# Optimization experiments

Measured on AMD Instinct MI355X. Metric: run time of the kernel, lower is better.

## Reference

```python
import jax, jax.numpy as jnp
import numpy as np

HIDDEN = 1280
HEADS = 8
RANK = 4
BATCH = 2
SEQ = 4096


def setup_inputs() -> dict:
    key = jax.random.key(0)
    ks = jax.random.split(key, 11)
    s = 1.0 / np.sqrt(HIDDEN)
    return {
        "hidden_states": jax.random.normal(ks[0], (BATCH, SEQ, HIDDEN), jnp.float32),
        # attn projections (stored as [in, out] for x @ W)
        "w_q": jax.random.normal(ks[1], (HIDDEN, HIDDEN), jnp.float32) * s,
        "w_k": jax.random.normal(ks[2], (HIDDEN, HIDDEN), jnp.float32) * s,
        "w_v": jax.random.normal(ks[3], (HIDDEN, HIDDEN), jnp.float32) * s,
        # LoRA down/up matrices for K and V
        "lora_k_a": jax.random.normal(ks[4], (HIDDEN, RANK), jnp.float32) * s,
        "lora_k_b": jax.random.normal(ks[5], (RANK, HIDDEN), jnp.float32) * 0.5,
        "lora_v_a": jax.random.normal(ks[6], (HIDDEN, RANK), jnp.float32) * s,
        "lora_v_b": jax.random.normal(ks[7], (RANK, HIDDEN), jnp.float32) * 0.5,
        # output projection (to_out[0]); to_out[1] is dropout -> identity at eval
        "w_out": jax.random.normal(ks[8], (HIDDEN, HIDDEN), jnp.float32) * s,
        "b_out": jax.random.normal(ks[9], (HIDDEN,), jnp.float32) * 0.01,
    }


def reference(hidden_states, w_q, w_k, w_v, lora_k_a, lora_k_b,
              lora_v_a, lora_v_b, w_out, b_out):
    B, S, D = hidden_states.shape
    H = HEADS
    dh = D // H
    scale = 1.0 / np.sqrt(dh)

    # QKV projections
    q = hidden_states @ w_q                      # [B, S, D]
    k = hidden_states @ w_k
    v = hidden_states @ w_v

    # LoRA low-rank residual updates to key/value
    k = k + (k @ lora_k_a) @ lora_k_b            # rank-4 update
    v = v + (v @ lora_v_a) @ lora_v_b

    # head_to_batch_dim: [B, S, D] -> [B, H, S, dh]
    q = q.reshape(B, S, H, dh).transpose(0, 2, 1, 3)
    k = k.reshape(B, S, H, dh).transpose(0, 2, 1, 3)
    v = v.reshape(B, S, H, dh).transpose(0, 2, 1, 3)

    # naive attention: scores -> softmax -> weighted sum
    scores = jnp.einsum("bhqd,bhkd->bhqk", q, k) * scale   # [B, H, S, S]
    probs = jax.nn.softmax(scores, axis=-1)
    out = jnp.einsum("bhqk,bhkd->bhqd", probs, v)          # [B, H, S, dh]

    # batch_to_head_dim: [B, H, S, dh] -> [B, S, D]
    out = out.transpose(0, 2, 1, 3).reshape(B, S, D)

    # to_out[0] linear; to_out[1] dropout is identity in eval
    return out @ w_out + b_out
```

## Files before the change

### kernel.cpp

```cpp
#include <hip/hip_runtime.h>
#include <stdint.h>

typedef __attribute__((ext_vector_type(8))) __bf16 bf16x8;
typedef __attribute__((ext_vector_type(2))) __bf16 bf16x2;
typedef __attribute__((ext_vector_type(4))) float f32x4;
typedef __attribute__((ext_vector_type(16))) float f32x16;
typedef unsigned short u16;

#define LOG2E 1.44269504088896f

static_assert(sizeof(bf16x8) == 16, "bf16x8 must be 16B");

__device__ __forceinline__ u16 f2bf(float f) {
  unsigned u = __builtin_bit_cast(unsigned, f);
  u += 0x7fffu + ((u >> 16) & 1u);
  return (u16)(u >> 16);
}

__device__ __forceinline__ void load_lds16(const void* g, void* l) {
  __builtin_amdgcn_global_load_lds((const __attribute__((address_space(1))) void*)g,
                                   (__attribute__((address_space(3))) void*)l, 16, 0, 0);
}

__global__ __launch_bounds__(256) void lora_tmp_k(
    const float* __restrict__ wk, const float* __restrict__ wv,
    const float* __restrict__ ka, const float* __restrict__ va,
    float* __restrict__ tk, float* __restrict__ tv) {
  const int i = blockIdx.x;
  const float* W = blockIdx.y ? wv : wk;
  const float* A = blockIdx.y ? va : ka;
  float* T = blockIdx.y ? tv : tk;
  float s0 = 0.f, s1 = 0.f, s2 = 0.f, s3 = 0.f;
  for (int j = threadIdx.x; j < 1280; j += 256) {
    float w = W[(size_t)i * 1280 + j];
    float4 a4 = *(const float4*)(A + (size_t)j * 4);
    s0 += w * a4.x; s1 += w * a4.y; s2 += w * a4.z; s3 += w * a4.w;
  }
#pragma unroll
  for (int m = 1; m < 64; m <<= 1) {
    s0 += __shfl_xor(s0, m); s1 += __shfl_xor(s1, m);
    s2 += __shfl_xor(s2, m); s3 += __shfl_xor(s3, m);
  }
  __shared__ float red[4][4];
  const int wv_ = threadIdx.x >> 6;
  if ((threadIdx.x & 63) == 0) {
    red[wv_][0] = s0; red[wv_][1] = s1; red[wv_][2] = s2; red[wv_][3] = s3;
  }
  __syncthreads();
  if (threadIdx.x < 4) {
    float r = red[0][threadIdx.x] + red[1][threadIdx.x] + red[2][threadIdx.x] + red[3][threadIdx.x];
    T[(size_t)i * 4 + threadIdx.x] = r;
  }
}

__global__ void wt_prep_k(const float* __restrict__ W, const float* __restrict__ tmp,
                          const float* __restrict__ LB, u16* __restrict__ WT) {
  __shared__ float tile[32][33];
  const int o0 = blockIdx.x * 32, i0 = blockIdx.y * 32;
  const int tx = threadIdx.x, ty = threadIdx.y;
#pragma unroll
  for (int kk = 0; kk < 4; ++kk) {
    int i = i0 + ty + kk * 8, o = o0 + tx;
    float v = W[(size_t)i * 1280 + o];
    if (tmp) {
      float4 t = *(const float4*)(tmp + (size_t)i * 4);
      v += t.x * LB[o] + t.y * LB[1280 + o] + t.z * LB[2560 + o] + t.w * LB[3840 + o];
    }
    tile[ty + kk * 8][tx] = v;
  }
  __syncthreads();
#pragma unroll
  for (int kk = 0; kk < 4; ++kk) {
    int o = o0 + ty + kk * 8, i = i0 + tx;
    WT[(size_t)o * 1280 + i] = f2bf(tile[tx][ty + kk * 8]);
  }
}

__global__ __launch_bounds__(256) void cvt_bf16_k(const float* __restrict__ in,
                                                  u16* __restrict__ out, int n4) {
  for (int i = blockIdx.x * 256 + threadIdx.x; i < n4; i += gridDim.x * 256) {
    float4 v = ((const float4*)in)[i];
    ushort4 o;
    o.x = f2bf(v.x); o.y = f2bf(v.y); o.z = f2bf(v.z); o.w = f2bf(v.w);
    ((ushort4*)out)[i] = o;
  }
}

__global__ void vtrans_k(const u16* __restrict__ V, u16* __restrict__ VT) {
  __shared__ u16 tile[32][33];
  const int s0 = blockIdx.x * 32, c0 = blockIdx.y * 32, b = blockIdx.z;
  const int tx = threadIdx.x, ty = threadIdx.y;
#pragma unroll
  for (int kk = 0; kk < 4; ++kk)
    tile[ty + kk * 8][tx] = V[(size_t)(b * 4096 + s0 + ty + kk * 8) * 1280 + c0 + tx];
  __syncthreads();
#pragma unroll
  for (int kk = 0; kk < 4; ++kk)
    VT[(size_t)(b * 1280 + c0 + ty + kk * 8) * 4096 + s0 + tx] = tile[tx][ty + kk * 8];
}

template <bool F32OUT>
__global__ __launch_bounds__(256) void gemm128_k(
    const u16* __restrict__ A, const u16* __restrict__ WT,
    void* __restrict__ outp, const float* __restrict__ bias, float oscale) {
  __shared__ __align__(16) u16 lds[2 * 128 * 40];
  u16* ldsA = lds;
  u16* ldsB = lds + 128 * 40;
  const int tid = threadIdx.x;
  const int lane = tid & 63, lrow = lane & 15, lhi = lane >> 4;
  const int w = tid >> 6, wm = w >> 1, wn = w & 1;
  const size_t M0 = (size_t)blockIdx.x * 128, N0 = (size_t)blockIdx.y * 128;
  const int wb = tid & 192;
  f32x4 acc[4][4] = {};

  for (int k0 = 0; k0 < 1280; k0 += 32) {
#pragma unroll
    for (int j = 0; j < 3; ++j) {
      if (j < 2 || tid < 128) {
        int i = j * 256 + tid;
        int row = i / 5, c = i % 5; c = c < 4 ? c : 3;
        load_lds16(A + (M0 + row) * 1280 + k0 + c * 8, ldsA + (j * 256 + wb) * 8);
      }
    }
#pragma unroll
    for (int j = 0; j < 3; ++j) {
      if (j < 2 || tid < 128) {
        int i = j * 256 + tid;
        int row = i / 5, c = i % 5; c = c < 4 ? c : 3;
        load_lds16(WT + (N0 + row) * 1280 + k0 + c * 8, ldsB + (j * 256 + wb) * 8);
      }
    }
    __syncthreads();
    bf16x8 af[4], bfr[4];
#pragma unroll
    for (int m = 0; m < 4; ++m)
      af[m] = *(const bf16x8*)(ldsA + (wm * 64 + m * 16 + lrow) * 40 + lhi * 8);
#pragma unroll
    for (int n = 0; n < 4; ++n)
      bfr[n] = *(const bf16x8*)(ldsB + (wn * 64 + n * 16 + lrow) * 40 + lhi * 8);
#pragma unroll
    for (int m = 0; m < 4; ++m)
#pragma unroll
      for (int n = 0; n < 4; ++n)
        acc[m][n] = __builtin_amdgcn_mfma_f32_16x16x32_bf16(af[m], bfr[n], acc[m][n], 0, 0, 0);
    __syncthreads();
  }

#pragma unroll
  for (int m = 0; m < 4; ++m)
#pragma unroll
    for (int n = 0; n < 4; ++n)
#pragma unroll
      for (int r = 0; r < 4; ++r) {
        size_t row = M0 + wm * 64 + m * 16 + lhi * 4 + r;
        size_t col = N0 + wn * 64 + n * 16 + lrow;
        float v = acc[m][n][r];
        if (F32OUT)
          ((float*)outp)[row * 1280 + col] = v + bias[col];
        else
          ((u16*)outp)[row * 1280 + col] = f2bf(v * oscale);
      }
}

__global__ __launch_bounds__(256, 2) void attn_k(
    const u16* __restrict__ Q, const u16* __restrict__ K,
    const u16* __restrict__ VT, u16* __restrict__ AO) {
  __shared__ __align__(16) u16 lds_all[34816];
  u16* const kb0 = lds_all;
  u16* const kb1 = lds_all + 12288;
  u16* const vt = lds_all + 24576;
  const int tid = threadIdx.x;
  const int lane = tid & 63;
  const int l31 = lane & 31, lhi5 = lane >> 5;
  const int lo32 = (lane < 32);
  const int w = tid >> 6;
  const int bh = blockIdx.x, qt = blockIdx.y;
  const int b = bh >> 3, h = bh & 7;
  const int wb = tid & 192;

  const u16* Kg = K + (size_t)b * 4096 * 1280 + h * 160;
  const u16* VTg = VT + ((size_t)b * 1280 + h * 160) * 4096;

  bf16x8 qf[10];
  const u16* Qg = Q + (size_t)(b * 4096 + qt * 128 + w * 32 + l31) * 1280 + h * 160 + lhi5 * 8;
#pragma unroll
  for (int kf = 0; kf < 10; ++kf) qf[kf] = *(const bf16x8*)(Qg + kf * 16);
#pragma unroll
  for (int kf = 0; kf < 10; ++kf) asm volatile("" : "+v"(qf[kf]));

  auto stageK = [&](int kv0, u16* dst) {
#pragma unroll
    for (int j = 0; j < 6; ++j) {
      int i = j * 256 + tid;
      int row = i / 24, cl = i % 24;
      int cg = (cl & 24) | ((cl ^ row) & 7);
      cg = cg < 20 ? cg : 19;
      load_lds16(Kg + (size_t)(kv0 + row) * 1280 + cg * 8, dst + (j * 256 + wb) * 8);
    }
  };
  auto stageV = [&](int kv0) {
#pragma unroll
    for (int j = 0; j < 5; ++j) {
      int i = j * 256 + tid;
      int row = i >> 3, cl = i & 7;
      int cg = cl ^ (row & 7);
      load_lds16(VTg + (size_t)row * 4096 + kv0 + cg * 8, vt + (j * 256 + wb) * 8);
    }
  };

  stageK(0, kb0);

  f32x16 o[5] = {};
  float m_run = -1e30f, l_run = 0.f;

  for (int t = 0; t < 64; ++t) {
    const u16* kcur = (t & 1) ? kb1 : kb0;
    u16* knext = (t & 1) ? kb0 : kb1;
    stageV(t * 64);
    if (t < 63) stageK((t + 1) * 64, knext);
    if (t < 63) { asm volatile("s_waitcnt vmcnt(11)" ::: "memory"); }
    else        { asm volatile("s_waitcnt vmcnt(5)" ::: "memory"); }
    __builtin_amdgcn_s_barrier();
    __builtin_amdgcn_sched_barrier(0);

    f32x16 sacc[2] = {};
    __builtin_amdgcn_s_setprio(1);
#pragma unroll
    for (int kf = 0; kf < 10; ++kf) {
      const int c = 2 * kf + lhi5;
#pragma unroll
      for (int mt = 0; mt < 2; ++mt) {
        const int row = mt * 32 + l31;
        const int slot = (c & 24) | ((c ^ row) & 7);
        bf16x8 ka = *(const bf16x8*)(kcur + row * 192 + slot * 8);
        sacc[mt] = __builtin_amdgcn_mfma_f32_32x32x16_bf16(ka, qf[kf], sacc[mt], 0, 0, 0);
      }
    }
    __builtin_amdgcn_s_setprio(0);

    float mx = -1e30f;
#pragma unroll
    for (int mt = 0; mt < 2; ++mt)
#pragma unroll
      for (int i = 0; i < 16; ++i) mx = fmaxf(mx, sacc[mt][i]);
    mx = fmaxf(mx, __shfl_xor(mx, 32));
    if (__any(mx - m_run > 8.0f)) {
      float mnew = fmaxf(m_run, mx);
      float al = __builtin_amdgcn_exp2f((m_run - mnew) * LOG2E);
      l_run *= al; m_run = mnew;
#pragma unroll
      for (int dm = 0; dm < 5; ++dm)
#pragma unroll
        for (int i = 0; i < 16; ++i) o[dm][i] *= al;
    }
    float rs = 0.f;
    unsigned xp[2][8];
#pragma unroll
    for (int mt = 0; mt < 2; ++mt)
#pragma unroll
      for (int r = 0; r < 8; ++r) {
        float p0 = __builtin_amdgcn_exp2f((sacc[mt][2 * r] - m_run) * LOG2E);
        float p1 = __builtin_amdgcn_exp2f((sacc[mt][2 * r + 1] - m_run) * LOG2E);
        rs += p0 + p1;
        bf16x2 pk; pk[0] = (__bf16)p0; pk[1] = (__bf16)p1;
        xp[mt][r] = __builtin_bit_cast(unsigned, pk);
      }
    rs += __shfl_xor(rs, 32);
    l_run += rs;

    if (t < 63) { asm volatile("s_waitcnt vmcnt(6)" ::: "memory"); }
    else        { asm volatile("s_waitcnt vmcnt(0)" ::: "memory"); }
    __builtin_amdgcn_s_barrier();
    __builtin_amdgcn_sched_barrier(0);

    __builtin_amdgcn_s_setprio(1);
#pragma unroll
    for (int kf = 0; kf < 4; ++kf) {
      const int mt = kf >> 1, hf = kf & 1;
      unsigned xa = xp[mt][hf * 4 + 0], xb = xp[mt][hf * 4 + 1];
      unsigned xc = xp[mt][hf * 4 + 2], xd = xp[mt][hf * 4 + 3];
      unsigned sa = __shfl_xor((int)xa, 32), sb = __shfl_xor((int)xb, 32);
      unsigned sc = __shfl_xor((int)xc, 32), sd = __shfl_xor((int)xd, 32);
      uint4 pw;
      pw.x = lo32 ? xa : sc;
      pw.y = lo32 ? xb : sd;
      pw.z = lo32 ? sa : xc;
      pw.w = lo32 ? sb : xd;
      bf16x8 pB = __builtin_bit_cast(bf16x8, pw);
      const int c = 2 * kf + lhi5;
#pragma unroll
      for (int dm = 0; dm < 5; ++dm) {
        const int row = dm * 32 + l31;
        bf16x8 va = *(const bf16x8*)(vt + row * 64 + ((c ^ (row & 7)) * 8));
        o[dm] = __builtin_amdgcn_mfma_f32_32x32x16_bf16(va, pB, o[dm], 0, 0, 0);
      }
    }
    __builtin_amdgcn_s_setprio(0);
    __builtin_amdgcn_sched_barrier(0);
    __builtin_amdgcn_s_barrier();
    __builtin_amdgcn_sched_barrier(0);
  }

  float invl = 1.f / l_run;
  u16* tr = lds_all + w * 5376;
#pragma unroll
  for (int dm = 0; dm < 5; ++dm)
#pragma unroll
    for (int k = 0; k < 4; ++k) {
      int d = dm * 32 + k * 8 + lhi5 * 4;
      unsigned lo_ = (unsigned)f2bf(o[dm][4 * k + 0] * invl) |
                     ((unsigned)f2bf(o[dm][4 * k + 1] * invl) << 16);
      unsigned hi_ = (unsigned)f2bf(o[dm][4 * k + 2] * invl) |
                     ((unsigned)f2bf(o[dm][4 * k + 3] * invl) << 16);
      uint2 u; u.x = lo_; u.y = hi_;
      *(uint2*)(tr + l31 * 168 + d) = u;
    }
  asm volatile("s_waitcnt lgkmcnt(0)" ::: "memory");
  __builtin_amdgcn_sched_barrier(0);
  const size_t qg0 = (size_t)(b * 4096 + qt * 128 + w * 32);
#pragma unroll
  for (int it = 0; it < 10; ++it) {
    int idx = it * 64 + lane;
    int row = idx / 20, cc = idx % 20;
    bf16x8 vch = *(const bf16x8*)(tr + row * 168 + cc * 8);
    *(bf16x8*)(AO + (qg0 + row) * 1280 + h * 160 + cc * 8) = vch;
  }
}

extern "C" void kernel_launch(void* const* d_in, const int* in_sizes, int n_in,
                              void* d_out, int out_size, void* d_ws, size_t ws_size,
                              hipStream_t stream) {
  const float* hs  = (const float*)d_in[0];
  const float* w_q = (const float*)d_in[1];
  const float* w_k = (const float*)d_in[2];
  const float* w_v = (const float*)d_in[3];
  const float* lka = (const float*)d_in[4];
  const float* lkb = (const float*)d_in[5];
  const float* lva = (const float*)d_in[6];
  const float* lvb = (const float*)d_in[7];
  const float* w_o = (const float*)d_in[8];
  const float* b_o = (const float*)d_in[9];
  float* out = (float*)d_out;
  char* ws = (char*)d_ws;

  const size_t KA  = 0;
  const size_t VA  = 20480;
  const size_t WTQ = 40960;
  const size_t WTK = WTQ + 3276800;
  const size_t WTV = WTK + 3276800;
  const size_t WTO = WTV + 3276800;
  const size_t HSB = WTO + 3276800;
  const size_t QB  = HSB + 20971520;
  const size_t KB  = QB + 20971520;
  const size_t VB  = KB + 20971520;
  const size_t VTB = VB + 20971520;
  const size_t AOB = VTB + 20971520;
  const size_t END = AOB + 20971520;
  if (ws_size < END) return;

  float* tk = (float*)(ws + KA);
  float* tv = (float*)(ws + VA);
  u16* wtq = (u16*)(ws + WTQ);
  u16* wtk = (u16*)(ws + WTK);
  u16* wtv = (u16*)(ws + WTV);
  u16* wto = (u16*)(ws + WTO);
  u16* hsb = (u16*)(ws + HSB);
  u16* qb  = (u16*)(ws + QB);
  u16* kb  = (u16*)(ws + KB);
  u16* vb  = (u16*)(ws + VB);
  u16* vtb = (u16*)(ws + VTB);
  u16* aob = (u16*)(ws + AOB);

  lora_tmp_k<<<dim3(1280, 2), 256, 0, stream>>>(w_k, w_v, lka, lva, tk, tv);
  wt_prep_k<<<dim3(40, 40), dim3(32, 8), 0, stream>>>(w_q, nullptr, nullptr, wtq);
  wt_prep_k<<<dim3(40, 40), dim3(32, 8), 0, stream>>>(w_k, tk, lkb, wtk);
  wt_prep_k<<<dim3(40, 40), dim3(32, 8), 0, stream>>>(w_v, tv, lvb, wtv);
  wt_prep_k<<<dim3(40, 40), dim3(32, 8), 0, stream>>>(w_o, nullptr, nullptr, wto);
  cvt_bf16_k<<<2048, 256, 0, stream>>>(hs, hsb, 2621440);

  const float qscale = 0.07905694150420949f;
  gemm128_k<false><<<dim3(64, 10), 256, 0, stream>>>(hsb, wtq, qb, nullptr, qscale);
  gemm128_k<false><<<dim3(64, 10), 256, 0, stream>>>(hsb, wtk, kb, nullptr, 1.0f);
  gemm128_k<false><<<dim3(64, 10), 256, 0, stream>>>(hsb, wtv, vb, nullptr, 1.0f);
  vtrans_k<<<dim3(128, 40, 2), dim3(32, 8), 0, stream>>>(vb, vtb);
  attn_k<<<dim3(16, 32), 256, 0, stream>>>(qb, kb, vtb, aob);
  gemm128_k<true><<<dim3(64, 10), 256, 0, stream>>>(aob, wto, (void*)out, b_o, 1.0f);
}
```

Before: 383.8 us.

## Double-buffer V tiles, compact K LDS layout, and drop trailing barrier

Each iteration now prefetches both the next K and V tiles into alternating LDS buffers, so V loads overlap the current tile's compute instead of being issued the same iteration they are used. The K tile LDS stride shrinks from 192 to 160 elements with a new swizzle for the last column groups, which frees space for the second V buffer. The per-iteration end barrier is removed and the loop is unrolled by two. The softmax max/sum reductions become trees with split accumulators, and the exponent uses an fmaf with a precomputed scaled max. Removing the end barrier may let a fast wave overwrite a V buffer that slower waves are still reading for the P·V step.

```diff
diff --git a/kernel.cpp b/kernel.cpp
--- a/kernel.cpp
+++ b/kernel.cpp
@@ -165,10 +165,11 @@
 __global__ __launch_bounds__(256, 2) void attn_k(
     const u16* __restrict__ Q, const u16* __restrict__ K,
     const u16* __restrict__ VT, u16* __restrict__ AO) {
-  __shared__ __align__(16) u16 lds_all[34816];
+  __shared__ __align__(16) u16 lds_all[40960];
   u16* const kb0 = lds_all;
-  u16* const kb1 = lds_all + 12288;
-  u16* const vt = lds_all + 24576;
+  u16* const kb1 = lds_all + 10240;
+  u16* const vt0 = lds_all + 20480;
+  u16* const vt1 = lds_all + 30720;
   const int tid = threadIdx.x;
   const int lane = tid & 63;
   const int l31 = lane & 31, lhi5 = lane >> 5;
@@ -190,36 +191,35 @@
 
   auto stageK = [&](int kv0, u16* dst) {
 #pragma unroll
-    for (int j = 0; j < 6; ++j) {
+    for (int j = 0; j < 5; ++j) {
       int i = j * 256 + tid;
-      int row = i / 24, cl = i % 24;
-      int cg = (cl & 24) | ((cl ^ row) & 7);
-      cg = cg < 20 ? cg : 19;
+      int row = i / 20, cl = i % 20;
+      int cg = (cl < 16) ? ((cl & 24) | ((cl ^ row) & 7))
+                         : (16 + ((cl ^ (row >> 1)) & 3));
       load_lds16(Kg + (size_t)(kv0 + row) * 1280 + cg * 8, dst + (j * 256 + wb) * 8);
     }
   };
-  auto stageV = [&](int kv0) {
+  auto stageV = [&](int kv0, u16* dst) {
 #pragma unroll
     for (int j = 0; j < 5; ++j) {
       int i = j * 256 + tid;
       int row = i >> 3, cl = i & 7;
       int cg = cl ^ (row & 7);
-      load_lds16(VTg + (size_t)row * 4096 + kv0 + cg * 8, vt + (j * 256 + wb) * 8);
+      load_lds16(VTg + (size_t)row * 4096 + kv0 + cg * 8, dst + (j * 256 + wb) * 8);
     }
   };
 
   stageK(0, kb0);
+  stageV(0, vt0);
 
   f32x16 o[5] = {};
   float m_run = -1e30f, l_run = 0.f;
-
-  for (int t = 0; t < 64; ++t) {
-    const u16* kcur = (t & 1) ? kb1 : kb0;
-    u16* knext = (t & 1) ? kb0 : kb1;
-    stageV(t * 64);
-    if (t < 63) stageK((t + 1) * 64, knext);
-    if (t < 63) { asm volatile("s_waitcnt vmcnt(11)" ::: "memory"); }
-    else        { asm volatile("s_waitcnt vmcnt(5)" ::: "memory"); }
+  float mLog = m_run * LOG2E;
+
+  auto body = [&](int t, const u16* kcur, const u16* vcur, u16* knx, u16* vnx, bool last) {
+    if (!last) { stageK((t + 1) * 64, knx); stageV((t + 1) * 64, vnx); }
+    if (!last) { asm volatile("s_waitcnt vmcnt(15)" ::: "memory"); }
+    else       { asm volatile("s_waitcnt vmcnt(5)" ::: "memory"); }
     __builtin_amdgcn_s_barrier();
     __builtin_amdgcn_sched_barrier(0);
 
@@ -231,45 +231,52 @@
 #pragma unroll
       for (int mt = 0; mt < 2; ++mt) {
         const int row = mt * 32 + l31;
-        const int slot = (c & 24) | ((c ^ row) & 7);
-        bf16x8 ka = *(const bf16x8*)(kcur + row * 192 + slot * 8);
+        const int slot = (kf < 8) ? ((c & 24) | ((c ^ row) & 7))
+                                  : (16 + ((c ^ (row >> 1)) & 3));
+        bf16x8 ka = *(const bf16x8*)(kcur + row * 160 + slot * 8);
         sacc[mt] = __builtin_amdgcn_mfma_f32_32x32x16_bf16(ka, qf[kf], sacc[mt], 0, 0, 0);
       }
     }
     __builtin_amdgcn_s_setprio(0);
 
-    float mx = -1e30f;
-#pragma unroll
-    for (int mt = 0; mt < 2; ++mt)
-#pragma unroll
-      for (int i = 0; i < 16; ++i) mx = fmaxf(mx, sacc[mt][i]);
+    float tmx[8];
+#pragma unroll
+    for (int i = 0; i < 8; ++i)
+      tmx[i] = fmaxf(fmaxf(sacc[0][i], sacc[0][i + 8]),
+                     fmaxf(sacc[1][i], sacc[1][i + 8]));
+    float mx = fmaxf(fmaxf(fmaxf(tmx[0], tmx[1]), fmaxf(tmx[2], tmx[3])),
+                     fmaxf(fmaxf(tmx[4], tmx[5]), fmaxf(tmx[6], tmx[7])));
     mx = fmaxf(mx, __shfl_xor(mx, 32));
     if (__any(mx - m_run > 8.0f)) {
       float mnew = fmaxf(m_run, mx);
       float al = __builtin_amdgcn_exp2f((m_run - mnew) * LOG2E);
-      l_run *= al; m_run = mnew;
+      l_run *= al; m_run = mnew; mLog = m_run * LOG2E;
 #pragma unroll
       for (int dm = 0; dm < 5; ++dm)
 #pragma unroll
         for (int i = 0; i < 16; ++i) o[dm][i] *= al;
     }
-    float rs = 0.f;
+    float rs0 = 0.f, rs1 = 0.f, rs2 = 0.f, rs3 = 0.f;
     unsigned xp[2][8];
 #pragma unroll
     for (int mt = 0; mt < 2; ++mt)
 #pragma unroll
       for (int r = 0; r < 8; ++r) {
-        float p0 = __builtin_amdgcn_exp2f((sacc[mt][2 * r] - m_run) * LOG2E);
-        float p1 = __builtin_amdgcn_exp2f((sacc[mt][2 * r + 1] - m_run) * LOG2E);
-        rs += p0 + p1;
+        float p0 = __builtin_amdgcn_exp2f(fmaf(sacc[mt][2 * r], LOG2E, -mLog));
+        float p1 = __builtin_amdgcn_exp2f(fmaf(sacc[mt][2 * r + 1], LOG2E, -mLog));
+        if ((r & 3) == 0) rs0 += p0 + p1;
+        else if ((r & 3) == 1) rs1 += p0 + p1;
+        else if ((r & 3) == 2) rs2 += p0 + p1;
+        else rs3 += p0 + p1;
         bf16x2 pk; pk[0] = (__bf16)p0; pk[1] = (__bf16)p1;
         xp[mt][r] = __builtin_bit_cast(unsigned, pk);
       }
+    float rs = (rs0 + rs1) + (rs2 + rs3);
     rs += __shfl_xor(rs, 32);
     l_run += rs;
 
-    if (t < 63) { asm volatile("s_waitcnt vmcnt(6)" ::: "memory"); }
-    else        { asm volatile("s_waitcnt vmcnt(0)" ::: "memory"); }
+    if (!last) { asm volatile("s_waitcnt vmcnt(10)" ::: "memory"); }
+    else       { asm volatile("s_waitcnt vmcnt(0)" ::: "memory"); }
     __builtin_amdgcn_s_barrier();
     __builtin_amdgcn_sched_barrier(0);
 
@@ -291,15 +298,19 @@
 #pragma unroll
       for (int dm = 0; dm < 5; ++dm) {
         const int row = dm * 32 + l31;
-        bf16x8 va = *(const bf16x8*)(vt + row * 64 + ((c ^ (row & 7)) * 8));
+        bf16x8 va = *(const bf16x8*)(vcur + row * 64 + ((c ^ (row & 7)) * 8));
         o[dm] = __builtin_amdgcn_mfma_f32_32x32x16_bf16(va, pB, o[dm], 0, 0, 0);
       }
     }
     __builtin_amdgcn_s_setprio(0);
-    __builtin_amdgcn_sched_barrier(0);
-    __builtin_amdgcn_s_barrier();
-    __builtin_amdgcn_sched_barrier(0);
-  }
+  };
+
+  for (int t = 0; t < 62; t += 2) {
+    body(t, kb0, vt0, kb1, vt1, false);
+    body(t + 1, kb1, vt1, kb0, vt0, false);
+  }
+  body(62, kb0, vt0, kb1, vt1, false);
+  body(63, kb1, vt1, kb0, vt0, true);
 
   float invl = 1.f / l_run;
   u16* tr = lds_all + w * 5376;
```

Result: slower. 394.8 us (+2.9%).
